# Performance work log

Measured on AMD Instinct MI355X. Metric: run time of the kernel, lower is better.

Reference implementation:

```python
import jax, jax.numpy as jnp
import numpy as np

D = 1024  # input_dim


def setup_inputs() -> dict:
    key = jax.random.key(0)
    ks = jax.random.split(key, 7)
    scale = 1.0 / np.sqrt(D)
    x = jax.random.normal(ks[0], (4, D, 2048), dtype=jnp.float32)
    Wq = jax.random.uniform(ks[1], (D, D), jnp.float32, -scale, scale)
    bq = jax.random.uniform(ks[2], (D,), jnp.float32, -scale, scale)
    Wk = jax.random.uniform(ks[3], (D, D), jnp.float32, -scale, scale)
    bk = jax.random.uniform(ks[4], (D,), jnp.float32, -scale, scale)
    Wv = jax.random.uniform(ks[5], (D, D), jnp.float32, -scale, scale)
    bv = jax.random.uniform(ks[6], (D,), jnp.float32, -scale, scale)
    return {"x": x, "Wq": Wq, "bq": bq, "Wk": Wk, "bk": bk, "Wv": Wv, "bv": bv}


def reference(x, Wq, bq, Wk, bk, Wv, bv):
    # x: [B, D, S] -> [B, S, D]
    xt = jnp.transpose(x, (0, 2, 1))
    # torch nn.Linear: y = x @ W^T + b
    q = jnp.einsum('bsd,ed->bse', xt, Wq) + bq
    k = jnp.einsum('bsd,ed->bse', xt, Wk) + bk
    v = jnp.einsum('bsd,ed->bse', xt, Wv) + bv
    scores = jnp.einsum('bse,bte->bst', q, k) / jnp.sqrt(jnp.float32(D))
    attn = jax.nn.softmax(scores, axis=2)
    out = jnp.einsum('bst,bte->bse', attn, v)  # [B, S, D]
    return out
```

## Files before the change

kernel.cpp:

```cpp
#include <hip/hip_runtime.h>
#include <stdint.h>

typedef unsigned short us16;
typedef unsigned short us8  __attribute__((ext_vector_type(8)));
typedef unsigned short us4v __attribute__((ext_vector_type(4)));
typedef __bf16         bf16x8 __attribute__((ext_vector_type(8)));
typedef float          f32x4  __attribute__((ext_vector_type(4)));

__device__ __forceinline__ us16 f2bf(float f) {
    union { float f; unsigned int u; } c; c.f = f;
    unsigned int u = (c.u + 0x7fffu + ((c.u >> 16) & 1u)) >> 16;
    return (us16)u;
}
__device__ __forceinline__ float bf2f(us16 h) {
    union { unsigned int u; float f; } c; c.u = ((unsigned int)h) << 16;
    return c.f;
}

__device__ __forceinline__ void async16(const us16* g, us16* l) {
    __builtin_amdgcn_global_load_lds(
        (const __attribute__((address_space(1))) unsigned int*)g,
        (__attribute__((address_space(3))) unsigned int*)l,
        16, 0, 0);
}

template <int EPI>
__device__ __forceinline__ void gemm_core(
        const us16* __restrict__ A, const us16* __restrict__ B,
        void* __restrict__ C, const float* __restrict__ bias,
        float* __restrict__ L,
        int M, int K, int x, int y, us16* lsA, us16* lsB) {
    const int m0 = x * 128, n0 = y * 128;
    const int tid = threadIdx.x;
    const int lane = tid & 63, wid = tid >> 6;
    const int l15 = lane & 15, quad = lane >> 4;
    const int wm = (wid & 1) * 64, wn = (wid >> 1) * 64;

    f32x4 acc[4][4] = {};

    const int srow = wid * 32 + (lane >> 3);
    const int sc8 = (lane & 7) ^ ((lane >> 3) & 7);
    const us16* Ap = A + (size_t)(m0 + srow) * K + sc8 * 8;
    const us16* Bp = B + (size_t)(n0 + srow) * K + sc8 * 8;
    us16* ldsAw = &lsA[(wid * 32) * 64];
    us16* ldsBw = &lsB[(wid * 32) * 64];

    for (int kb = 0; kb < K; kb += 64) {
        __syncthreads();
#pragma unroll
        for (int c = 0; c < 4; c++) {
            async16(Ap + kb + (size_t)(c * 8) * K, ldsAw + c * 8 * 64);
            async16(Bp + kb + (size_t)(c * 8) * K, ldsBw + c * 8 * 64);
        }
        __syncthreads();
#pragma unroll
        for (int ks = 0; ks < 2; ks++) {
            bf16x8 af[4], bfr[4];
#pragma unroll
            for (int i = 0; i < 4; i++) {
                const int ra = wm + i * 16 + l15;
                const int rb = wn + i * 16 + l15;
                const int pa = ((ks * 4 + quad) ^ (ra & 7)) * 8;
                const int pb = ((ks * 4 + quad) ^ (rb & 7)) * 8;
                af[i]  = *(const bf16x8*)(&lsA[ra * 64 + pa]);
                bfr[i] = *(const bf16x8*)(&lsB[rb * 64 + pb]);
            }
#pragma unroll
            for (int i = 0; i < 4; i++)
#pragma unroll
                for (int j = 0; j < 4; j++)
                    acc[i][j] = __builtin_amdgcn_mfma_f32_16x16x32_bf16(af[i], bfr[j], acc[i][j], 0, 0, 0);
        }
    }

    if (EPI == 2) {
        const float scale = 0.03125f;
        float rs[4] = {0.f, 0.f, 0.f, 0.f};
#pragma unroll
        for (int i = 0; i < 4; i++) {
            const int mb = m0 + wm + i * 16 + quad * 4;
#pragma unroll
            for (int j = 0; j < 4; j++) {
                const int n = n0 + wn + j * 16 + l15;
                f32x4 v = acc[i][j];
                const float e0 = __expf(v[0] * scale), e1 = __expf(v[1] * scale);
                const float e2 = __expf(v[2] * scale), e3 = __expf(v[3] * scale);
                rs[j] += (e0 + e1) + (e2 + e3);
                us4v st = { f2bf(e0), f2bf(e1), f2bf(e2), f2bf(e3) };
                *(us4v*)((us16*)C + (size_t)n * M + mb) = st;
            }
        }
#pragma unroll
        for (int j = 0; j < 4; j++) {
            rs[j] += __shfl_xor(rs[j], 16, 64);
            rs[j] += __shfl_xor(rs[j], 32, 64);
        }
        if (quad == 0) {
#pragma unroll
            for (int j = 0; j < 4; j++)
                atomicAdd(&L[n0 + wn + j * 16 + l15], rs[j]);
        }
        return;
    }

#pragma unroll
    for (int i = 0; i < 4; i++) {
        const int mb = m0 + wm + i * 16 + quad * 4;
        float b0 = 0.f, b1 = 0.f, b2 = 0.f, b3 = 0.f;
        if (EPI == 0) {
            float4 bv4 = *(const float4*)(bias + mb);
            b0 = bv4.x; b1 = bv4.y; b2 = bv4.z; b3 = bv4.w;
        }
#pragma unroll
        for (int j = 0; j < 4; j++) {
            const int n = n0 + wn + j * 16 + l15;
            f32x4 v = acc[i][j];
            if (EPI == 3) {
                const float inv = 1.0f / L[n];
                float4 st;
                st.x = v[0] * inv; st.y = v[1] * inv;
                st.z = v[2] * inv; st.w = v[3] * inv;
                *(float4*)((float*)C + (size_t)n * M + mb) = st;
            } else {
                const float bn = (EPI == 1) ? bias[n] : 0.0f;
                us4v st = { f2bf(v[0] + b0 + bn), f2bf(v[1] + b1 + bn),
                            f2bf(v[2] + b2 + bn), f2bf(v[3] + b3 + bn) };
                *(us4v*)((us16*)C + (size_t)n * M + mb) = st;
            }
        }
    }
}

__device__ __forceinline__ void strip_xy(int lin, int gy, int& x, int& y) {
    const int within = lin & (4 * gy - 1);
    x = (lin / (4 * gy)) * 4 + (within & 3);
    y = within >> 2;
}

__global__ __launch_bounds__(256)
void prep(const float* __restrict__ x, us16* __restrict__ xt,
          const float* __restrict__ wq, const float* __restrict__ wk,
          const float* __restrict__ wv, us16* __restrict__ wb) {
    __shared__ us16 tile[64 * 65];
    const int id = blockIdx.x;
    const int t = threadIdx.x;
    if (id < 2048) {
        const int s0 = (id & 31) * 64, d0 = ((id >> 5) & 15) * 64, b = id >> 9;
        const float* xp = x + ((size_t)b * 1024 + d0) * 2048 + s0;
        const int r = t >> 4, c4 = t & 15;
#pragma unroll
        for (int i = 0; i < 4; i++) {
            float4 v = *(const float4*)(xp + (size_t)(r + 16 * i) * 2048 + c4 * 4);
            const int d = r + 16 * i;
            tile[(c4 * 4 + 0) * 65 + d] = f2bf(v.x);
            tile[(c4 * 4 + 1) * 65 + d] = f2bf(v.y);
            tile[(c4 * 4 + 2) * 65 + d] = f2bf(v.z);
            tile[(c4 * 4 + 3) * 65 + d] = f2bf(v.w);
        }
        __syncthreads();
        us16* op = xt + ((size_t)b * 2048 + s0) * 1024 + d0;
#pragma unroll
        for (int i = 0; i < 2; i++) {
            const int u = t + 256 * i;
            const int s = u >> 3, c8 = u & 7;
            us8 o;
#pragma unroll
            for (int j = 0; j < 8; j++) o[j] = tile[s * 65 + c8 * 8 + j];
            *(us8*)(op + (size_t)s * 1024 + c8 * 8) = o;
        }
    } else {
        const int cid = id - 2048;
        const int mb = cid >> 10;
        const float* src = (mb == 0) ? wq : (mb == 1) ? wk : wv;
        const size_t off = ((size_t)(cid & 1023) * 256 + t) * 4;
        float4 v = *(const float4*)(src + off);
        us4v o = { f2bf(v.x), f2bf(v.y), f2bf(v.z), f2bf(v.w) };
        *(us4v*)(wb + (size_t)mb * 1048576 + off) = o;
    }
}

__global__ __launch_bounds__(256)
void qkv(const us16* __restrict__ Wb, const us16* __restrict__ XT,
         us16* __restrict__ Qb, us16* __restrict__ Kb, us16* __restrict__ VT,
         const float* __restrict__ bq, const float* __restrict__ bk,
         const float* __restrict__ bv) {
    __shared__ us16 lsA[128 * 64];
    __shared__ us16 lsB[128 * 64];
    const int id = blockIdx.x;
    const long long sXT = 2097152;
    if (id < 1024) {
        const int z = id >> 7, zz = z & 3;
        const bool isK = z >= 4;
        int x, y; strip_xy(id & 127, 16, x, y);
        const us16* A = Wb + (isK ? 1048576 : 0);
        const us16* B = XT + (size_t)zz * sXT;
        us16* C = (isK ? Kb : Qb) + (size_t)zz * sXT;
        gemm_core<0>(A, B, (void*)C, isK ? bk : bq, nullptr, 1024, 1024, x, y, lsA, lsB);
    } else {
        const int id2 = id - 1024;
        const int z = id2 >> 7;
        int x, y; strip_xy(id2 & 127, 8, x, y);
        const us16* A = XT + (size_t)z * sXT;
        us16* C = VT + (size_t)z * sXT;
        gemm_core<1>(A, Wb + 2097152, (void*)C, bv, nullptr, 2048, 1024, x, y, lsA, lsB);
    }
}

__global__ __launch_bounds__(256)
void scores_k(const us16* __restrict__ Kb, const us16* __restrict__ Qb,
              us16* __restrict__ Sb, float* __restrict__ L) {
    __shared__ us16 lsA[128 * 64];
    __shared__ us16 lsB[128 * 64];
    const long long sXT = 2097152, sSS = 4194304;
    const int z = blockIdx.z;
    int x, y; strip_xy(blockIdx.x + 16 * blockIdx.y, 16, x, y);
    gemm_core<2>(Kb + (size_t)z * sXT, Qb + (size_t)z * sXT,
                 (void*)(Sb + (size_t)z * sSS), nullptr, L + z * 2048,
                 2048, 1024, x, y, lsA, lsB);
}

__global__ __launch_bounds__(256)
void out_k(const us16* __restrict__ VT, const us16* __restrict__ Sb,
           float* __restrict__ L, float* __restrict__ out) {
    __shared__ us16 lsA[128 * 64];
    __shared__ us16 lsB[128 * 64];
    const long long sXT = 2097152, sSS = 4194304;
    const int z = blockIdx.z;
    int x, y; strip_xy(blockIdx.x + 8 * blockIdx.y, 16, x, y);
    gemm_core<3>(VT + (size_t)z * sXT, Sb + (size_t)z * sSS,
                 (void*)(out + (size_t)z * sXT), nullptr, L + z * 2048,
                 1024, 2048, x, y, lsA, lsB);
}

extern "C" void kernel_launch(void* const* d_in, const int* in_sizes, int n_in,
                              void* d_out, int out_size, void* d_ws, size_t ws_size,
                              hipStream_t stream) {
    const float* x  = (const float*)d_in[0];
    const float* Wq = (const float*)d_in[1];
    const float* bq = (const float*)d_in[2];
    const float* Wk = (const float*)d_in[3];
    const float* bk = (const float*)d_in[4];
    const float* Wv = (const float*)d_in[5];
    const float* bv = (const float*)d_in[6];
    float* out = (float*)d_out;
    char* ws = (char*)d_ws;

    const size_t SZ = 16777216;
    us16* Qb = (us16*)(ws);
    us16* Kb = (us16*)(ws + SZ);
    us16* VT = (us16*)(ws + 2 * SZ);
    us16* XT = (us16*)(ws + 3 * SZ);
    us16* Wb = (us16*)(ws + 4 * SZ);
    us16* Sb = (us16*)(ws + 3 * SZ);
    float* Lb = (float*)(ws + 5 * SZ);

    dim3 blk(256, 1, 1);

    hipMemsetAsync(Lb, 0, 4 * 2048 * sizeof(float), stream);
    prep<<<dim3(5120, 1, 1), blk, 0, stream>>>(x, XT, Wq, Wk, Wv, Wb);
    qkv<<<dim3(1536, 1, 1), blk, 0, stream>>>(Wb, XT, Qb, Kb, VT, bq, bk, bv);
    scores_k<<<dim3(16, 16, 4), blk, 0, stream>>>(Kb, Qb, Sb, Lb);
    out_k<<<dim3(8, 16, 4), blk, 0, stream>>>(VT, Sb, Lb, out);
}
```

Baseline: 246.3 us.

## Fuse four kernels into one persistent kernel with grid barriers

Replaces the separate prep, QKV, scores and output launches with a single kernel of 1024 blocks that loops over work units and synchronises stages through an atomic grid-wide barrier. The aim is to remove kernel-launch gaps and the tail of each stage. It relies on all 1024 blocks being co-resident (launch bounds of 4 blocks per CU), otherwise the barrier can deadlock. Stages with fewer units than blocks leave some blocks idle, and the QKV stage now runs in two uneven rounds.

```diff
diff --git a/kernel.cpp b/kernel.cpp
--- a/kernel.cpp
+++ b/kernel.cpp
@@ -12,16 +12,25 @@
     unsigned int u = (c.u + 0x7fffu + ((c.u >> 16) & 1u)) >> 16;
     return (us16)u;
 }
-__device__ __forceinline__ float bf2f(us16 h) {
-    union { unsigned int u; float f; } c; c.u = ((unsigned int)h) << 16;
-    return c.f;
-}
 
 __device__ __forceinline__ void async16(const us16* g, us16* l) {
     __builtin_amdgcn_global_load_lds(
         (const __attribute__((address_space(1))) unsigned int*)g,
         (__attribute__((address_space(3))) unsigned int*)l,
         16, 0, 0);
+}
+
+__device__ __forceinline__ void grid_barrier(unsigned* bar, int phase) {
+    __syncthreads();
+    if (threadIdx.x == 0) {
+        __threadfence();
+        atomicAdd(bar, 1u);
+        const unsigned target = 1024u * (unsigned)(phase + 1);
+        while (__hip_atomic_load(bar, __ATOMIC_ACQUIRE,
+                                 __HIP_MEMORY_SCOPE_AGENT) < target)
+            __builtin_amdgcn_s_sleep(2);
+    }
+    __syncthreads();
 }
 
 template <int EPI>
@@ -137,99 +146,105 @@
     y = within >> 2;
 }
 
-__global__ __launch_bounds__(256)
-void prep(const float* __restrict__ x, us16* __restrict__ xt,
-          const float* __restrict__ wq, const float* __restrict__ wk,
-          const float* __restrict__ wv, us16* __restrict__ wb) {
-    __shared__ us16 tile[64 * 65];
-    const int id = blockIdx.x;
+__global__ __launch_bounds__(256, 4)
+void mega(const float* __restrict__ x,
+          const float* __restrict__ Wq, const float* __restrict__ bq,
+          const float* __restrict__ Wk, const float* __restrict__ bk,
+          const float* __restrict__ Wv, const float* __restrict__ bv,
+          float* __restrict__ out, char* __restrict__ ws) {
+    __shared__ us16 lsA[8192];
+    __shared__ us16 lsB[8192];
+
+    const size_t SZ = 16777216;
+    us16* Qb = (us16*)(ws);
+    us16* Kb = (us16*)(ws + SZ);
+    us16* VT = (us16*)(ws + 2 * SZ);
+    us16* XT = (us16*)(ws + 3 * SZ);
+    us16* Wb = (us16*)(ws + 4 * SZ);
+    us16* Sb = (us16*)(ws + 3 * SZ);
+    float* Lb = (float*)(ws + 5 * SZ);
+    unsigned* bar = (unsigned*)(ws + 5 * SZ + 32768);
+
+    const long long sXT = 2097152;
+    const long long sSS = 4194304;
+    const int bid = blockIdx.x;
     const int t = threadIdx.x;
-    if (id < 2048) {
-        const int s0 = (id & 31) * 64, d0 = ((id >> 5) & 15) * 64, b = id >> 9;
-        const float* xp = x + ((size_t)b * 1024 + d0) * 2048 + s0;
-        const int r = t >> 4, c4 = t & 15;
-#pragma unroll
-        for (int i = 0; i < 4; i++) {
-            float4 v = *(const float4*)(xp + (size_t)(r + 16 * i) * 2048 + c4 * 4);
-            const int d = r + 16 * i;
-            tile[(c4 * 4 + 0) * 65 + d] = f2bf(v.x);
-            tile[(c4 * 4 + 1) * 65 + d] = f2bf(v.y);
-            tile[(c4 * 4 + 2) * 65 + d] = f2bf(v.z);
-            tile[(c4 * 4 + 3) * 65 + d] = f2bf(v.w);
+
+    for (int u = bid; u < 5120; u += 1024) {
+        if (u < 2048) {
+            us16* tile = lsA;
+            const int s0 = (u & 31) * 64, d0 = ((u >> 5) & 15) * 64, b = u >> 9;
+            const float* xp = x + ((size_t)b * 1024 + d0) * 2048 + s0;
+            const int r = t >> 4, c4 = t & 15;
+#pragma unroll
+            for (int i = 0; i < 4; i++) {
+                float4 v = *(const float4*)(xp + (size_t)(r + 16 * i) * 2048 + c4 * 4);
+                const int d = r + 16 * i;
+                tile[(c4 * 4 + 0) * 65 + d] = f2bf(v.x);
+                tile[(c4 * 4 + 1) * 65 + d] = f2bf(v.y);
+                tile[(c4 * 4 + 2) * 65 + d] = f2bf(v.z);
+                tile[(c4 * 4 + 3) * 65 + d] = f2bf(v.w);
+            }
+            __syncthreads();
+            us16* op = XT + ((size_t)b * 2048 + s0) * 1024 + d0;
+#pragma unroll
+            for (int i = 0; i < 2; i++) {
+                const int uu = t + 256 * i;
+                const int s = uu >> 3, c8 = uu & 7;
+                us8 o;
+#pragma unroll
+                for (int j = 0; j < 8; j++) o[j] = tile[s * 65 + c8 * 8 + j];
+                *(us8*)(op + (size_t)s * 1024 + c8 * 8) = o;
+            }
+        } else {
+            const int cid = u - 2048;
+            const int mb = cid >> 10;
+            const float* src = (mb == 0) ? Wq : (mb == 1) ? Wk : Wv;
+            const size_t off = ((size_t)(cid & 1023) * 256 + t) * 4;
+            float4 v = *(const float4*)(src + off);
+            us4v o = { f2bf(v.x), f2bf(v.y), f2bf(v.z), f2bf(v.w) };
+            *(us4v*)(Wb + (size_t)mb * 1048576 + off) = o;
         }
         __syncthreads();
-        us16* op = xt + ((size_t)b * 2048 + s0) * 1024 + d0;
-#pragma unroll
-        for (int i = 0; i < 2; i++) {
-            const int u = t + 256 * i;
-            const int s = u >> 3, c8 = u & 7;
-            us8 o;
-#pragma unroll
-            for (int j = 0; j < 8; j++) o[j] = tile[s * 65 + c8 * 8 + j];
-            *(us8*)(op + (size_t)s * 1024 + c8 * 8) = o;
-        }
-    } else {
-        const int cid = id - 2048;
-        const int mb = cid >> 10;
-        const float* src = (mb == 0) ? wq : (mb == 1) ? wk : wv;
-        const size_t off = ((size_t)(cid & 1023) * 256 + t) * 4;
-        float4 v = *(const float4*)(src + off);
-        us4v o = { f2bf(v.x), f2bf(v.y), f2bf(v.z), f2bf(v.w) };
-        *(us4v*)(wb + (size_t)mb * 1048576 + off) = o;
-    }
-}
-
-__global__ __launch_bounds__(256)
-void qkv(const us16* __restrict__ Wb, const us16* __restrict__ XT,
-         us16* __restrict__ Qb, us16* __restrict__ Kb, us16* __restrict__ VT,
-         const float* __restrict__ bq, const float* __restrict__ bk,
-         const float* __restrict__ bv) {
-    __shared__ us16 lsA[128 * 64];
-    __shared__ us16 lsB[128 * 64];
-    const int id = blockIdx.x;
-    const long long sXT = 2097152;
-    if (id < 1024) {
-        const int z = id >> 7, zz = z & 3;
-        const bool isK = z >= 4;
-        int x, y; strip_xy(id & 127, 16, x, y);
-        const us16* A = Wb + (isK ? 1048576 : 0);
-        const us16* B = XT + (size_t)zz * sXT;
-        us16* C = (isK ? Kb : Qb) + (size_t)zz * sXT;
-        gemm_core<0>(A, B, (void*)C, isK ? bk : bq, nullptr, 1024, 1024, x, y, lsA, lsB);
-    } else {
-        const int id2 = id - 1024;
-        const int z = id2 >> 7;
-        int x, y; strip_xy(id2 & 127, 8, x, y);
-        const us16* A = XT + (size_t)z * sXT;
-        us16* C = VT + (size_t)z * sXT;
-        gemm_core<1>(A, Wb + 2097152, (void*)C, bv, nullptr, 2048, 1024, x, y, lsA, lsB);
-    }
-}
-
-__global__ __launch_bounds__(256)
-void scores_k(const us16* __restrict__ Kb, const us16* __restrict__ Qb,
-              us16* __restrict__ Sb, float* __restrict__ L) {
-    __shared__ us16 lsA[128 * 64];
-    __shared__ us16 lsB[128 * 64];
-    const long long sXT = 2097152, sSS = 4194304;
-    const int z = blockIdx.z;
-    int x, y; strip_xy(blockIdx.x + 16 * blockIdx.y, 16, x, y);
-    gemm_core<2>(Kb + (size_t)z * sXT, Qb + (size_t)z * sXT,
-                 (void*)(Sb + (size_t)z * sSS), nullptr, L + z * 2048,
-                 2048, 1024, x, y, lsA, lsB);
-}
-
-__global__ __launch_bounds__(256)
-void out_k(const us16* __restrict__ VT, const us16* __restrict__ Sb,
-           float* __restrict__ L, float* __restrict__ out) {
-    __shared__ us16 lsA[128 * 64];
-    __shared__ us16 lsB[128 * 64];
-    const long long sXT = 2097152, sSS = 4194304;
-    const int z = blockIdx.z;
-    int x, y; strip_xy(blockIdx.x + 8 * blockIdx.y, 16, x, y);
-    gemm_core<3>(VT + (size_t)z * sXT, Sb + (size_t)z * sSS,
-                 (void*)(out + (size_t)z * sXT), nullptr, L + z * 2048,
-                 1024, 2048, x, y, lsA, lsB);
+    }
+    grid_barrier(bar, 0);
+
+    for (int u = bid; u < 1536; u += 1024) {
+        if (u < 1024) {
+            const int z = u >> 7, zz = z & 3;
+            const bool isK = z >= 4;
+            int xx, yy; strip_xy(u & 127, 16, xx, yy);
+            const us16* A = Wb + (isK ? 1048576 : 0);
+            const us16* B = XT + (size_t)zz * sXT;
+            us16* C = (isK ? Kb : Qb) + (size_t)zz * sXT;
+            gemm_core<0>(A, B, (void*)C, isK ? bk : bq, nullptr, 1024, 1024, xx, yy, lsA, lsB);
+        } else {
+            const int u2 = u - 1024;
+            const int z = u2 >> 7;
+            int xx, yy; strip_xy(u2 & 127, 8, xx, yy);
+            gemm_core<1>(XT + (size_t)z * sXT, Wb + 2097152,
+                         (void*)(VT + (size_t)z * sXT), bv, nullptr,
+                         2048, 1024, xx, yy, lsA, lsB);
+        }
+    }
+    grid_barrier(bar, 1);
+
+    {
+        const int z = bid >> 8;
+        int xx, yy; strip_xy(bid & 255, 16, xx, yy);
+        gemm_core<2>(Kb + (size_t)z * sXT, Qb + (size_t)z * sXT,
+                     (void*)(Sb + (size_t)z * sSS), nullptr, Lb + z * 2048,
+                     2048, 1024, xx, yy, lsA, lsB);
+    }
+    grid_barrier(bar, 2);
+
+    if (bid < 512) {
+        const int z = bid >> 7;
+        int xx, yy; strip_xy(bid & 127, 16, xx, yy);
+        gemm_core<3>(VT + (size_t)z * sXT, Sb + (size_t)z * sSS,
+                     (void*)(out + (size_t)z * sXT), nullptr, Lb + z * 2048,
+                     1024, 2048, xx, yy, lsA, lsB);
+    }
 }
 
 extern "C" void kernel_launch(void* const* d_in, const int* in_sizes, int n_in,
@@ -246,19 +261,7 @@
     char* ws = (char*)d_ws;
 
     const size_t SZ = 16777216;
-    us16* Qb = (us16*)(ws);
-    us16* Kb = (us16*)(ws + SZ);
-    us16* VT = (us16*)(ws + 2 * SZ);
-    us16* XT = (us16*)(ws + 3 * SZ);
-    us16* Wb = (us16*)(ws + 4 * SZ);
-    us16* Sb = (us16*)(ws + 3 * SZ);
-    float* Lb = (float*)(ws + 5 * SZ);
-
-    dim3 blk(256, 1, 1);
-
-    hipMemsetAsync(Lb, 0, 4 * 2048 * sizeof(float), stream);
-    prep<<<dim3(5120, 1, 1), blk, 0, stream>>>(x, XT, Wq, Wk, Wv, Wb);
-    qkv<<<dim3(1536, 1, 1), blk, 0, stream>>>(Wb, XT, Qb, Kb, VT, bq, bk, bv);
-    scores_k<<<dim3(16, 16, 4), blk, 0, stream>>>(Kb, Qb, Sb, Lb);
-    out_k<<<dim3(8, 16, 4), blk, 0, stream>>>(VT, Sb, Lb, out);
-}
+    hipMemsetAsync(ws + 5 * SZ, 0, 32768 + 64, stream);
+    mega<<<dim3(1024, 1, 1), dim3(256, 1, 1), 0, stream>>>(
+        x, Wq, bq, Wk, bk, Wv, bv, out, ws);
+}
```

New measurement: 853.1 us. 246% more time.
